# Kernel tuning notes

Hardware: AMD Instinct MI355X
Metric: run time of the kernel (lower is better)

The kernel has to match this reference:

```python
import jax, jax.numpy as jnp
import numpy as np

N = 8192
F_IN = 512
F_OUT = 64
ALPHA = 0.2  # LeakyReLU negative slope
NEG_INF = -9e15


def setup_inputs() -> dict:
    key = jax.random.key(0)
    k1, k2, k3, k4 = jax.random.split(key, 4)
    inp = jax.random.normal(k1, (N, F_IN), dtype=jnp.float32)
    adj = jax.random.randint(k2, (N, N), 0, 2, dtype=jnp.int32)
    W = jax.random.normal(k3, (F_IN, F_OUT), dtype=jnp.float32) * 0.05
    a = jax.random.normal(k4, (2 * F_OUT, 1), dtype=jnp.float32) * 0.05
    return {"inp": inp, "adj": adj, "W": W, "a": a}


def reference(inp, adj, W, a):
    # h = W(inp): [N, F_OUT]
    h = inp @ W
    # a([h_i || h_j]) decomposes exactly into a1.h_i + a2.h_j, avoiding the
    # [N*N, 2F] concat tensor while computing identical math.
    f1 = h @ a[:F_OUT]        # [N, 1] source-node term
    f2 = h @ a[F_OUT:]        # [N, 1] target-node term
    e = jax.nn.leaky_relu(f1 + f2.T, negative_slope=ALPHA)  # [N, N]
    masked = jnp.where(adj > 0, e, jnp.float32(NEG_INF))
    attention = jax.nn.softmax(masked, axis=1)  # dropout is no-op at inference
    h_prime = attention @ h   # [N, F_OUT]
    return jax.nn.elu(h_prime)  # concat=True branch
```

## Files before the change

### kernel.cpp

```cpp
#include <hip/hip_runtime.h>

#define NN   8192
#define FIN  512
#define FOUT 64

typedef __attribute__((ext_vector_type(8))) short short8;
typedef __attribute__((ext_vector_type(4))) float floatx4;

__device__ __forceinline__ unsigned f2bf_u(float f) {
  union { float f; unsigned u; } v; v.f = f;
  return (v.u + 0x7fffu + ((v.u >> 16) & 1u)) >> 16;
}
__device__ __forceinline__ unsigned pack2(float a, float b) {
  return f2bf_u(a) | (f2bf_u(b) << 16);
}

__global__ __launch_bounds__(256) void k1_gemm_h(
    const float* __restrict__ inp, const float* __restrict__ W,
    const float* __restrict__ a,
    float* __restrict__ f1, float* __restrict__ f2,
    unsigned short* __restrict__ hT)
{
  __shared__ unsigned short at[32][72];
  __shared__ unsigned short wt[64][72];
  __shared__ float hsm[32][65];
  __shared__ float alds[2 * FOUT];

  const int tid   = threadIdx.x;
  const int rbase = blockIdx.x * 32;
  if (tid < 2 * FOUT) alds[tid] = a[tid];

  const int lane = tid & 63;
  const int wv   = tid >> 6;
  const int l15  = lane & 15;
  const int q    = lane >> 4;
  const int mi   = wv & 1;
  const int ni0  = (wv >> 1) * 2;

  const int r_a  = tid >> 3;
  const int k8   = (tid & 7) * 8;
  const int n_w  = tid & 63;
  const int kb_w = (tid >> 6) * 16;

  floatx4 acc0 = {0.f, 0.f, 0.f, 0.f};
  floatx4 acc1 = {0.f, 0.f, 0.f, 0.f};

  for (int kk0 = 0; kk0 < FIN; kk0 += 64) {
    __syncthreads();
    const float* ap = inp + (rbase + r_a) * FIN + kk0 + k8;
    float4 v0 = *(const float4*)ap;
    float4 v1 = *(const float4*)(ap + 4);
    *(uint4*)&at[r_a][k8] = make_uint4(pack2(v0.x, v0.y), pack2(v0.z, v0.w),
                                       pack2(v1.x, v1.y), pack2(v1.z, v1.w));
#pragma unroll
    for (int kk2 = 0; kk2 < 16; ++kk2)
      wt[n_w][kb_w + kk2] = (unsigned short)f2bf_u(W[(kk0 + kb_w + kk2) * FOUT + n_w]);
    __syncthreads();
#pragma unroll
    for (int ks = 0; ks < 2; ++ks) {
      short8 af = *(const short8*)&at[mi * 16 + l15][ks * 32 + q * 8];
      short8 b0 = *(const short8*)&wt[ni0 * 16 + l15][ks * 32 + q * 8];
      short8 b1 = *(const short8*)&wt[(ni0 + 1) * 16 + l15][ks * 32 + q * 8];
      acc0 = __builtin_amdgcn_mfma_f32_16x16x32_bf16(af, b0, acc0, 0, 0, 0);
      acc1 = __builtin_amdgcn_mfma_f32_16x16x32_bf16(af, b1, acc1, 0, 0, 0);
    }
  }

  {
    const int m0 = mi * 16 + q * 4;
    const int i0 = rbase + m0;
    {
      const int n = ni0 * 16 + l15;
#pragma unroll
      for (int rg = 0; rg < 4; ++rg) hsm[m0 + rg][n] = acc0[rg];
      *(uint2*)&hT[n * NN + i0] = make_uint2(pack2(acc0[0], acc0[1]),
                                             pack2(acc0[2], acc0[3]));
    }
    {
      const int n = (ni0 + 1) * 16 + l15;
#pragma unroll
      for (int rg = 0; rg < 4; ++rg) hsm[m0 + rg][n] = acc1[rg];
      *(uint2*)&hT[n * NN + i0] = make_uint2(pack2(acc1[0], acc1[1]),
                                             pack2(acc1[2], acc1[3]));
    }
  }
  __syncthreads();
  if (tid < 32) {
    float s1 = 0.f, s2 = 0.f;
#pragma unroll 8
    for (int c = 0; c < FOUT; ++c) {
      float hv = hsm[tid][c];
      s1 += hv * alds[c];
      s2 += hv * alds[FOUT + c];
    }
    f1[rbase + tid] = s1;
    f2[rbase + tid] = s2;
  }
}

__global__ __launch_bounds__(256) void k2_attn(
    const int* __restrict__ adj,
    const float* __restrict__ f1g, const float* __restrict__ f2g,
    const unsigned short* __restrict__ hT,
    float* __restrict__ out)
{
  __shared__ unsigned short wlds[16][136];
  __shared__ unsigned short hlds[64][136];
  __shared__ float lred[16][17];
  __shared__ float linv_s[16];

  const int tid   = threadIdx.x;
  const int rbase = blockIdx.x * 16;
  const int lane  = tid & 63;
  const int wv    = tid >> 6;
  const int l15   = lane & 15;
  const int q     = lane >> 4;

  const int r  = tid >> 4;
  const int c8 = (tid & 15) * 8;
  const float f1v = f1g[rbase + r];
  const int* arow = adj + (size_t)(rbase + r) * NN + c8;

  const int fh = tid >> 2;
  const int sg = (tid & 3) * 32;
  const unsigned short* hrow = hT + (size_t)fh * NN + sg;

  floatx4 acc = {0.f, 0.f, 0.f, 0.f};
  float lsum = 0.f;

  int4 A0, A1; float4 F0, F1; int4 H0, H1, H2, H3;
  A0 = *(const int4*)(arow);
  A1 = *(const int4*)(arow + 4);
  F0 = *(const float4*)(f2g + c8);
  F1 = *(const float4*)(f2g + c8 + 4);
  H0 = *(const int4*)(hrow);
  H1 = *(const int4*)(hrow + 8);
  H2 = *(const int4*)(hrow + 16);
  H3 = *(const int4*)(hrow + 24);

  for (int it = 0; it < 64; ++it) {
    __syncthreads();
    float e, w0, w1, w2, w3, w4, w5, w6, w7;
    e = f1v + F0.x; e = (e > 0.f) ? e : 0.2f * e; w0 = A0.x ? __expf(e) : 0.f;
    e = f1v + F0.y; e = (e > 0.f) ? e : 0.2f * e; w1 = A0.y ? __expf(e) : 0.f;
    e = f1v + F0.z; e = (e > 0.f) ? e : 0.2f * e; w2 = A0.z ? __expf(e) : 0.f;
    e = f1v + F0.w; e = (e > 0.f) ? e : 0.2f * e; w3 = A0.w ? __expf(e) : 0.f;
    e = f1v + F1.x; e = (e > 0.f) ? e : 0.2f * e; w4 = A1.x ? __expf(e) : 0.f;
    e = f1v + F1.y; e = (e > 0.f) ? e : 0.2f * e; w5 = A1.y ? __expf(e) : 0.f;
    e = f1v + F1.z; e = (e > 0.f) ? e : 0.2f * e; w6 = A1.z ? __expf(e) : 0.f;
    e = f1v + F1.w; e = (e > 0.f) ? e : 0.2f * e; w7 = A1.w ? __expf(e) : 0.f;
    lsum += ((w0 + w1) + (w2 + w3)) + ((w4 + w5) + (w6 + w7));
    *(uint4*)&wlds[r][c8] = make_uint4(pack2(w0, w1), pack2(w2, w3),
                                       pack2(w4, w5), pack2(w6, w7));
    *(int4*)&hlds[fh][sg]      = H0;
    *(int4*)&hlds[fh][sg + 8]  = H1;
    *(int4*)&hlds[fh][sg + 16] = H2;
    *(int4*)&hlds[fh][sg + 24] = H3;
    __syncthreads();
    if (it < 63) {
      const int kk = (it + 1) * 128;
      A0 = *(const int4*)(arow + kk);
      A1 = *(const int4*)(arow + kk + 4);
      F0 = *(const float4*)(f2g + kk + c8);
      F1 = *(const float4*)(f2g + kk + c8 + 4);
      H0 = *(const int4*)(hrow + kk);
      H1 = *(const int4*)(hrow + kk + 8);
      H2 = *(const int4*)(hrow + kk + 16);
      H3 = *(const int4*)(hrow + kk + 24);
    }
#pragma unroll
    for (int ks = 0; ks < 4; ++ks) {
      short8 af = *(const short8*)&wlds[l15][ks * 32 + q * 8];
      short8 bf = *(const short8*)&hlds[wv * 16 + l15][ks * 32 + q * 8];
      acc = __builtin_amdgcn_mfma_f32_16x16x32_bf16(af, bf, acc, 0, 0, 0);
    }
  }

  lred[r][tid & 15] = lsum;
  __syncthreads();
  if (tid < 16) {
    float s = 0.f;
#pragma unroll
    for (int i = 0; i < 16; ++i) s += lred[tid][i];
    linv_s[tid] = 1.f / s;
  }
  __syncthreads();

  const int m0  = q * 4;
  const int nn2 = wv * 16 + l15;
#pragma unroll
  for (int rg = 0; rg < 4; ++rg) {
    float v = acc[rg] * linv_s[m0 + rg];
    v = (v > 0.f) ? v : (__expf(v) - 1.f);
    out[(size_t)(rbase + m0 + rg) * FOUT + nn2] = v;
  }
}

extern "C" void kernel_launch(void* const* d_in, const int* in_sizes, int n_in,
                              void* d_out, int out_size, void* d_ws, size_t ws_size,
                              hipStream_t stream) {
  (void)in_sizes; (void)n_in; (void)out_size; (void)ws_size;
  const float* inp = (const float*)d_in[0];
  const int*   adj = (const int*)d_in[1];
  const float* W   = (const float*)d_in[2];
  const float* a   = (const float*)d_in[3];
  float* out = (float*)d_out;

  float* f1 = (float*)d_ws;
  float* f2 = f1 + NN;
  unsigned short* hT = (unsigned short*)(f2 + NN);

  k1_gemm_h<<<NN / 32, 256, 0, stream>>>(inp, W, a, f1, f2, hT);
  k2_attn<<<NN / 16, 256, 0, stream>>>(adj, f1, f2, hT, out);
}
```

Before: 389.1 us.

## Restructure both kernels: register-resident operands, double-buffered LDS, larger K tiles

The projection kernel now stages all of W in LDS once, uses 16-row blocks, and feeds the input matrix straight from registers into MFMA with a two-deep prefetch. The attention kernel doubles the K tile to 256 and keeps the h operand in registers loaded directly from global memory, so the h LDS staging is gone. It also double-buffers the weight tile in LDS, which leaves one barrier per iteration instead of two. The aim is to cut synchronization and LDS traffic and overlap the adjacency streaming with compute, at the cost of more registers and possibly lower occupancy.

After: 390.9 us. About the same (+0.5%).

```diff
diff --git a/kernel.cpp b/kernel.cpp
--- a/kernel.cpp
+++ b/kernel.cpp
@@ -3,6 +3,7 @@
 #define NN   8192
 #define FIN  512
 #define FOUT 64
+#define KT   256
 
 typedef __attribute__((ext_vector_type(8))) short short8;
 typedef __attribute__((ext_vector_type(4))) float floatx4;
@@ -14,6 +15,8 @@
 __device__ __forceinline__ unsigned pack2(float a, float b) {
   return f2bf_u(a) | (f2bf_u(b) << 16);
 }
+
+union U8 { uint4 u; short8 s; };
 
 __global__ __launch_bounds__(256) void k1_gemm_h(
     const float* __restrict__ inp, const float* __restrict__ W,
@@ -21,71 +24,79 @@
     float* __restrict__ f1, float* __restrict__ f2,
     unsigned short* __restrict__ hT)
 {
-  __shared__ unsigned short at[32][72];
-  __shared__ unsigned short wt[64][72];
-  __shared__ float hsm[32][65];
+  __shared__ unsigned short wt[64][520];
+  __shared__ float hsm[16][65];
   __shared__ float alds[2 * FOUT];
 
   const int tid   = threadIdx.x;
-  const int rbase = blockIdx.x * 32;
+  const int rbase = blockIdx.x * 16;
   if (tid < 2 * FOUT) alds[tid] = a[tid];
+
+  {
+    const float4* Wv = (const float4*)W;
+#pragma unroll
+    for (int j = 0; j < 32; ++j) {
+      const int i  = j * 256 + tid;
+      const int k  = i >> 4;
+      const int c4 = (i & 15) * 4;
+      float4 f = Wv[i];
+      wt[c4 + 0][k] = (unsigned short)f2bf_u(f.x);
+      wt[c4 + 1][k] = (unsigned short)f2bf_u(f.y);
+      wt[c4 + 2][k] = (unsigned short)f2bf_u(f.z);
+      wt[c4 + 3][k] = (unsigned short)f2bf_u(f.w);
+    }
+  }
 
   const int lane = tid & 63;
   const int wv   = tid >> 6;
   const int l15  = lane & 15;
   const int q    = lane >> 4;
-  const int mi   = wv & 1;
-  const int ni0  = (wv >> 1) * 2;
-
-  const int r_a  = tid >> 3;
-  const int k8   = (tid & 7) * 8;
-  const int n_w  = tid & 63;
-  const int kb_w = (tid >> 6) * 16;
-
-  floatx4 acc0 = {0.f, 0.f, 0.f, 0.f};
-  floatx4 acc1 = {0.f, 0.f, 0.f, 0.f};
-
-  for (int kk0 = 0; kk0 < FIN; kk0 += 64) {
-    __syncthreads();
-    const float* ap = inp + (rbase + r_a) * FIN + kk0 + k8;
-    float4 v0 = *(const float4*)ap;
-    float4 v1 = *(const float4*)(ap + 4);
-    *(uint4*)&at[r_a][k8] = make_uint4(pack2(v0.x, v0.y), pack2(v0.z, v0.w),
-                                       pack2(v1.x, v1.y), pack2(v1.z, v1.w));
-#pragma unroll
-    for (int kk2 = 0; kk2 < 16; ++kk2)
-      wt[n_w][kb_w + kk2] = (unsigned short)f2bf_u(W[(kk0 + kb_w + kk2) * FOUT + n_w]);
-    __syncthreads();
-#pragma unroll
-    for (int ks = 0; ks < 2; ++ks) {
-      short8 af = *(const short8*)&at[mi * 16 + l15][ks * 32 + q * 8];
-      short8 b0 = *(const short8*)&wt[ni0 * 16 + l15][ks * 32 + q * 8];
-      short8 b1 = *(const short8*)&wt[(ni0 + 1) * 16 + l15][ks * 32 + q * 8];
-      acc0 = __builtin_amdgcn_mfma_f32_16x16x32_bf16(af, b0, acc0, 0, 0, 0);
-      acc1 = __builtin_amdgcn_mfma_f32_16x16x32_bf16(af, b1, acc1, 0, 0, 0);
+
+  const float* ap = inp + (size_t)(rbase + l15) * FIN + q * 8;
+
+  float4 Ab[2][4];
+#pragma unroll
+  for (int b = 0; b < 2; ++b) {
+    Ab[b][0] = *(const float4*)(ap + b * 64);
+    Ab[b][1] = *(const float4*)(ap + b * 64 + 4);
+    Ab[b][2] = *(const float4*)(ap + b * 64 + 32);
+    Ab[b][3] = *(const float4*)(ap + b * 64 + 36);
+  }
+
+  floatx4 acc = {0.f, 0.f, 0.f, 0.f};
+  __syncthreads();
+
+#pragma unroll
+  for (int t = 0; t < 8; ++t) {
+    const int cur = t & 1;
+    U8 c0, c1;
+    c0.u = make_uint4(pack2(Ab[cur][0].x, Ab[cur][0].y), pack2(Ab[cur][0].z, Ab[cur][0].w),
+                      pack2(Ab[cur][1].x, Ab[cur][1].y), pack2(Ab[cur][1].z, Ab[cur][1].w));
+    c1.u = make_uint4(pack2(Ab[cur][2].x, Ab[cur][2].y), pack2(Ab[cur][2].z, Ab[cur][2].w),
+                      pack2(Ab[cur][3].x, Ab[cur][3].y), pack2(Ab[cur][3].z, Ab[cur][3].w));
+    if (t < 6) {
+      const float* an = ap + (t + 2) * 64;
+      Ab[cur][0] = *(const float4*)(an);
+      Ab[cur][1] = *(const float4*)(an + 4);
+      Ab[cur][2] = *(const float4*)(an + 32);
+      Ab[cur][3] = *(const float4*)(an + 36);
     }
-  }
-
-  {
-    const int m0 = mi * 16 + q * 4;
-    const int i0 = rbase + m0;
-    {
-      const int n = ni0 * 16 + l15;
-#pragma unroll
-      for (int rg = 0; rg < 4; ++rg) hsm[m0 + rg][n] = acc0[rg];
-      *(uint2*)&hT[n * NN + i0] = make_uint2(pack2(acc0[0], acc0[1]),
-                                             pack2(acc0[2], acc0[3]));
-    }
-    {
-      const int n = (ni0 + 1) * 16 + l15;
-#pragma unroll
-      for (int rg = 0; rg < 4; ++rg) hsm[m0 + rg][n] = acc1[rg];
-      *(uint2*)&hT[n * NN + i0] = make_uint2(pack2(acc1[0], acc1[1]),
-                                             pack2(acc1[2], acc1[3]));
-    }
-  }
-  __syncthreads();
-  if (tid < 32) {
+    const unsigned short* wrow = &wt[wv * 16 + l15][t * 64 + q * 8];
+    short8 b0 = *(const short8*)(wrow);
+    short8 b1 = *(const short8*)(wrow + 32);
+    acc = __builtin_amdgcn_mfma_f32_16x16x32_bf16(c0.s, b0, acc, 0, 0, 0);
+    acc = __builtin_amdgcn_mfma_f32_16x16x32_bf16(c1.s, b1, acc, 0, 0, 0);
+  }
+
+  const int m0 = q * 4;
+  const int n  = wv * 16 + l15;
+#pragma unroll
+  for (int rg = 0; rg < 4; ++rg) hsm[m0 + rg][n] = acc[rg];
+  *(uint2*)&hT[(size_t)n * NN + rbase + m0] =
+      make_uint2(pack2(acc[0], acc[1]), pack2(acc[2], acc[3]));
+
+  __syncthreads();
+  if (tid < 16) {
     float s1 = 0.f, s2 = 0.f;
 #pragma unroll 8
     for (int c = 0; c < FOUT; ++c) {
@@ -98,14 +109,62 @@
   }
 }
 
+#define GAT_W4(FV, AV, P0, P1)                                              \
+  { float e0 = f1v + FV.x; e0 = fmaxf(e0, 0.2f * e0);                       \
+    float e1 = f1v + FV.y; e1 = fmaxf(e1, 0.2f * e1);                       \
+    float e2 = f1v + FV.z; e2 = fmaxf(e2, 0.2f * e2);                       \
+    float e3 = f1v + FV.w; e3 = fmaxf(e3, 0.2f * e3);                       \
+    float x0 = AV.x ? __expf(e0) : 0.f;                                     \
+    float x1 = AV.y ? __expf(e1) : 0.f;                                     \
+    float x2 = AV.z ? __expf(e2) : 0.f;                                     \
+    float x3 = AV.w ? __expf(e3) : 0.f;                                     \
+    lsum += (x0 + x1) + (x2 + x3);                                          \
+    P0 = pack2(x0, x1); P1 = pack2(x2, x3); }
+
+#define K2_ITER(IT, ACUR, ANXT, BUF)                                        \
+  {                                                                          \
+    if ((IT) < 31) {   \
+      const int* apf = arow + ((IT) + 1) * KT;                               \
+      ANXT[0] = *(const int4*)(apf);                                         \
+      ANXT[1] = *(const int4*)(apf + 4);                                     \
+      ANXT[2] = *(const int4*)(apf + 8);                                     \
+      ANXT[3] = *(const int4*)(apf + 12);                                    \
+    }                                                                        \
+    unsigned p0, p1, p2, p3, p4, p5, p6, p7;                                 \
+    GAT_W4(F[0], ACUR[0], p0, p1)                                            \
+    GAT_W4(F[1], ACUR[1], p2, p3)                                            \
+    GAT_W4(F[2], ACUR[2], p4, p5)                                            \
+    GAT_W4(F[3], ACUR[3], p6, p7)                                            \
+    *(uint4*)&wlds[BUF][r][c16]     = make_uint4(p0, p1, p2, p3);            \
+    *(uint4*)&wlds[BUF][r][c16 + 8] = make_uint4(p4, p5, p6, p7);            \
+    if ((IT) < 31) {       \
+      const float* fpf = frow + ((IT) + 1) * KT;                             \
+      F[0] = *(const float4*)(fpf);                                          \
+      F[1] = *(const float4*)(fpf + 4);                                      \
+      F[2] = *(const float4*)(fpf + 8);                                      \
+      F[3] = *(const float4*)(fpf + 12);                                     \
+    }                                                                        \
+    asm volatile("s_waitcnt lgkmcnt(0)" ::: "memory");     \
+    __builtin_amdgcn_s_barrier();       \
+    _Pragma("unroll")                                                        \
+    for (int ks = 0; ks < 8; ++ks) {                                         \
+      short8 af = *(const short8*)&wlds[BUF][l15][ks * 32 + q * 8];          \
+      acc = __builtin_amdgcn_mfma_f32_16x16x32_bf16(af, Hf[ks], acc, 0, 0, 0); \
+    }                                                                        \
+    if ((IT) < 31) {                \
+      const unsigned short* hpf = hrow + ((IT) + 1) * KT;                    \
+      _Pragma("unroll")                                                      \
+      for (int ks = 0; ks < 8; ++ks) Hf[ks] = *(const short8*)(hpf + ks * 32); \
+    }                                                                        \
+  }
+
 __global__ __launch_bounds__(256) void k2_attn(
     const int* __restrict__ adj,
     const float* __restrict__ f1g, const float* __restrict__ f2g,
     const unsigned short* __restrict__ hT,
     float* __restrict__ out)
 {
-  __shared__ unsigned short wlds[16][136];
-  __shared__ unsigned short hlds[64][136];
+  __shared__ unsigned short wlds[2][16][264];
   __shared__ float lred[16][17];
   __shared__ float linv_s[16];
 
@@ -116,64 +175,34 @@
   const int l15   = lane & 15;
   const int q     = lane >> 4;
 
-  const int r  = tid >> 4;
-  const int c8 = (tid & 15) * 8;
+  const int r   = tid >> 4;
+  const int c16 = (tid & 15) * 16;
   const float f1v = f1g[rbase + r];
-  const int* arow = adj + (size_t)(rbase + r) * NN + c8;
-
-  const int fh = tid >> 2;
-  const int sg = (tid & 3) * 32;
-  const unsigned short* hrow = hT + (size_t)fh * NN + sg;
+  const int* arow   = adj + (size_t)(rbase + r) * NN + c16;
+  const float* frow = f2g + c16;
+  const unsigned short* hrow = hT + (size_t)(wv * 16 + l15) * NN + q * 8;
 
   floatx4 acc = {0.f, 0.f, 0.f, 0.f};
   float lsum = 0.f;
 
-  int4 A0, A1; float4 F0, F1; int4 H0, H1, H2, H3;
-  A0 = *(const int4*)(arow);
-  A1 = *(const int4*)(arow + 4);
-  F0 = *(const float4*)(f2g + c8);
-  F1 = *(const float4*)(f2g + c8 + 4);
-  H0 = *(const int4*)(hrow);
-  H1 = *(const int4*)(hrow + 8);
-  H2 = *(const int4*)(hrow + 16);
-  H3 = *(const int4*)(hrow + 24);
-
-  for (int it = 0; it < 64; ++it) {
-    __syncthreads();
-    float e, w0, w1, w2, w3, w4, w5, w6, w7;
-    e = f1v + F0.x; e = (e > 0.f) ? e : 0.2f * e; w0 = A0.x ? __expf(e) : 0.f;
-    e = f1v + F0.y; e = (e > 0.f) ? e : 0.2f * e; w1 = A0.y ? __expf(e) : 0.f;
-    e = f1v + F0.z; e = (e > 0.f) ? e : 0.2f * e; w2 = A0.z ? __expf(e) : 0.f;
-    e = f1v + F0.w; e = (e > 0.f) ? e : 0.2f * e; w3 = A0.w ? __expf(e) : 0.f;
-    e = f1v + F1.x; e = (e > 0.f) ? e : 0.2f * e; w4 = A1.x ? __expf(e) : 0.f;
-    e = f1v + F1.y; e = (e > 0.f) ? e : 0.2f * e; w5 = A1.y ? __expf(e) : 0.f;
-    e = f1v + F1.z; e = (e > 0.f) ? e : 0.2f * e; w6 = A1.z ? __expf(e) : 0.f;
-    e = f1v + F1.w; e = (e > 0.f) ? e : 0.2f * e; w7 = A1.w ? __expf(e) : 0.f;
-    lsum += ((w0 + w1) + (w2 + w3)) + ((w4 + w5) + (w6 + w7));
-    *(uint4*)&wlds[r][c8] = make_uint4(pack2(w0, w1), pack2(w2, w3),
-                                       pack2(w4, w5), pack2(w6, w7));
-    *(int4*)&hlds[fh][sg]      = H0;
-    *(int4*)&hlds[fh][sg + 8]  = H1;
-    *(int4*)&hlds[fh][sg + 16] = H2;
-    *(int4*)&hlds[fh][sg + 24] = H3;
-    __syncthreads();
-    if (it < 63) {
-      const int kk = (it + 1) * 128;
-      A0 = *(const int4*)(arow + kk);
-      A1 = *(const int4*)(arow + kk + 4);
-      F0 = *(const float4*)(f2g + kk + c8);
-      F1 = *(const float4*)(f2g + kk + c8 + 4);
-      H0 = *(const int4*)(hrow + kk);
-      H1 = *(const int4*)(hrow + kk + 8);
-      H2 = *(const int4*)(hrow + kk + 16);
-      H3 = *(const int4*)(hrow + kk + 24);
-    }
-#pragma unroll
-    for (int ks = 0; ks < 4; ++ks) {
-      short8 af = *(const short8*)&wlds[l15][ks * 32 + q * 8];
-      short8 bf = *(const short8*)&hlds[wv * 16 + l15][ks * 32 + q * 8];
-      acc = __builtin_amdgcn_mfma_f32_16x16x32_bf16(af, bf, acc, 0, 0, 0);
-    }
+  int4 Aa[4], Az[4];
+  float4 F[4];
+  short8 Hf[8];
+
+  Aa[0] = *(const int4*)(arow);
+  Aa[1] = *(const int4*)(arow + 4);
+  Aa[2] = *(const int4*)(arow + 8);
+  Aa[3] = *(const int4*)(arow + 12);
+  F[0] = *(const float4*)(frow);
+  F[1] = *(const float4*)(frow + 4);
+  F[2] = *(const float4*)(frow + 8);
+  F[3] = *(const float4*)(frow + 12);
+#pragma unroll
+  for (int ks = 0; ks < 8; ++ks) Hf[ks] = *(const short8*)(hrow + ks * 32);
+
+  for (int it = 0; it < 32; it += 2) {
+    K2_ITER(it,     Aa, Az, 0)
+    K2_ITER(it + 1, Az, Aa, 1)
   }
 
   lred[r][tid & 15] = lsum;
@@ -186,13 +215,13 @@
   }
   __syncthreads();
 
-  const int m0  = q * 4;
-  const int nn2 = wv * 16 + l15;
+  const int m0 = q * 4;
+  const int n2 = wv * 16 + l15;
 #pragma unroll
   for (int rg = 0; rg < 4; ++rg) {
     float v = acc[rg] * linv_s[m0 + rg];
     v = (v > 0.f) ? v : (__expf(v) - 1.f);
-    out[(size_t)(rbase + m0 + rg) * FOUT + nn2] = v;
+    out[(size_t)(rbase + m0 + rg) * FOUT + n2] = v;
   }
 }
 
@@ -210,6 +239,6 @@
   float* f2 = f1 + NN;
   unsigned short* hT = (unsigned short*)(f2 + NN);
 
-  k1_gemm_h<<<NN / 32, 256, 0, stream>>>(inp, W, a, f1, f2, hT);
+  k1_gemm_h<<<NN / 16, 256, 0, stream>>>(inp, W, a, f1, f2, hT);
   k2_attn<<<NN / 16, 256, 0, stream>>>(adj, f1, f2, hT, out);
 }
```
